# Optimization experiments

Measured on AMD Instinct MI355X. Metric: run time of the kernel, lower is better.

## Reference

```python
import jax, jax.numpy as jnp
import numpy as np

B, E, N = 8, 256, 32          # triples, padded edges per triple, neighbors per edge
D, RD = 512, 768              # graph_dim, relation-semantic dim
R = 2000                      # num relations
L = 2                         # relation-context layers
K = 8                         # top_k neighbor similarity
M, HEADS = 32, 8              # memory tokens, memory-attention heads
HLLM = 4096                   # llm hidden size
EPS = 1e-5


def _ln(x, g, b):
    mu = jnp.mean(x, -1, keepdims=True)
    var = jnp.mean(jnp.square(x - mu), -1, keepdims=True)
    return (x - mu) * jax.lax.rsqrt(var + EPS) * g + b


def setup_inputs() -> dict:
    key = jax.random.key(0)
    ks = iter(jax.random.split(key, 40))
    nrm = lambda shape, s=0.02: jax.random.normal(next(ks), shape, jnp.float32) * s
    return {
        'edge_rel_ids': jax.random.randint(next(ks), (B, E), 0, R, jnp.int32),
        'neighbor_rel_ids': jax.random.randint(next(ks), (B, E, N), 0, R, jnp.int32),
        'edge_mask': jnp.ones((B, E), jnp.float32),
        'rel_emb': nrm((R, RD), 1.0),
        'rp_w': nrm((D, RD)), 'rp_b': jnp.zeros((D,), jnp.float32),
        'ly_vw': nrm((L, D, D)), 'ly_vb': jnp.zeros((L, D), jnp.float32),
        'ly_ow': nrm((L, D, D)), 'ly_ob': jnp.zeros((L, D), jnp.float32),
        'ly_n1g': jnp.ones((L, D), jnp.float32), 'ly_n1b': jnp.zeros((L, D), jnp.float32),
        'ly_n2g': jnp.ones((L, D), jnp.float32), 'ly_n2b': jnp.zeros((L, D), jnp.float32),
        'ly_w1': nrm((L, 4 * D, D)), 'ly_b1': jnp.zeros((L, 4 * D), jnp.float32),
        'ly_w2': nrm((L, D, 4 * D)), 'ly_b2': jnp.zeros((L, D), jnp.float32),
        'mem_q': nrm((M, D)),
        't_qw': nrm((D, D)), 't_qb': jnp.zeros((D,), jnp.float32),
        't_kw': nrm((D, D)), 't_kb': jnp.zeros((D,), jnp.float32),
        't_vw': nrm((D, D)), 't_vb': jnp.zeros((D,), jnp.float32),
        't_ow': nrm((D, D)), 't_ob': jnp.zeros((D,), jnp.float32),
        'proj_w': nrm((HLLM, D)), 'proj_b': jnp.zeros((HLLM,), jnp.float32),
    }


def reference(edge_rel_ids, neighbor_rel_ids, edge_mask, rel_emb, rp_w, rp_b,
              ly_vw, ly_vb, ly_ow, ly_ob, ly_n1g, ly_n1b, ly_n2g, ly_n2b,
              ly_w1, ly_b1, ly_w2, ly_b2, mem_q,
              t_qw, t_qb, t_kw, t_kb, t_vw, t_vb, t_ow, t_ob, proj_w, proj_b):
    rel_vector = lambda ids: rel_emb[ids] @ rp_w.T + rp_b  # embedding gather + rel_proj
    rel_vec = rel_vector(edge_rel_ids)            # [B,E,D]
    neigh = rel_vector(neighbor_rel_ids)          # [B,E,N,D] dominant gather traffic
    # per-edge cosine similarity to neighbor relations, top-k mean aggregation
    rn = rel_vec / jnp.maximum(jnp.linalg.norm(rel_vec, axis=-1, keepdims=True), 1e-12)
    nn_ = neigh / jnp.maximum(jnp.linalg.norm(neigh, axis=-1, keepdims=True), 1e-12)
    sims = jnp.einsum('bend,bed->ben', nn_, rn)   # [B,E,N]
    _, top_idx = jax.lax.top_k(sims, K)           # [B,E,K]
    agg = jnp.take_along_axis(neigh, top_idx[..., None], axis=2).mean(axis=2)  # [B,E,D]
    # RelationContextLayer stack. Each layer attends from one edge-state token to a
    # single context token: softmax over one key is identically 1, so the MHA
    # reduces exactly to out_proj(v_proj(context)) -- same math as torch MHA here.
    states = rel_vec
    for l in range(L):
        attn = (agg @ ly_vw[l].T + ly_vb[l]) @ ly_ow[l].T + ly_ob[l]
        states = _ln(states + attn, ly_n1g[l], ly_n1b[l])
        ff = jax.nn.gelu(states @ ly_w1[l].T + ly_b1[l], approximate=False) @ ly_w2[l].T + ly_b2[l]
        states = _ln(states + ff, ly_n2g[l], ly_n2b[l])
        states = states * edge_mask[..., None]
    # GraphMemoryTokenizer: learned queries cross-attend over padded edge states
    dh = D // HEADS
    q = (mem_q @ t_qw.T + t_qb).reshape(M, HEADS, dh)
    k = (states @ t_kw.T + t_kb).reshape(B, E, HEADS, dh)
    v = (states @ t_vw.T + t_vb).reshape(B, E, HEADS, dh)
    scores = jnp.einsum('mhd,behd->bhme', q, k) / jnp.sqrt(jnp.asarray(dh, q.dtype))
    scores = jnp.where(edge_mask[:, None, None, :] == 0, jnp.finfo(scores.dtype).min, scores)
    attnw = jax.nn.softmax(scores, axis=-1)
    mem = jnp.einsum('bhme,behd->bmhd', attnw, v).reshape(B, M, D)
    mem = mem @ t_ow.T + t_ob
    no_edges = jnp.sum(edge_mask, axis=1) == 0    # rows with zero edges -> zero memory
    mem = jnp.where(no_edges[:, None, None], 0.0, mem)
    return mem @ proj_w.T + proj_b                # [B,M,HLLM]
```

## Files before the change

kernel.cpp:

```cpp
#include <hip/hip_runtime.h>
#include <hip/hip_bf16.h>
#include <math.h>

#define B_   8
#define E_   256
#define N_   32
#define D_   512
#define RD_  768
#define R_   2000
#define L_   2
#define K_   8
#define M_   32
#define H_   8
#define DH_  64
#define HL_  4096

typedef float f32x4 __attribute__((ext_vector_type(4)));
typedef __bf16 bf16x8 __attribute__((ext_vector_type(8)));
typedef const __attribute__((address_space(1))) void GVoid;
typedef __attribute__((address_space(3))) void LVoid;

__device__ __forceinline__ float gelu_exact(float x) {
    return 0.5f * x * (1.0f + erff(x * 0.70710678118654752f));
}
__device__ __forceinline__ unsigned short f2bf(float x) {
    return __hip_bfloat16_raw(__float2bfloat16(x)).x;
}

template <int TM, int TN, int ACT_GELU, int OUT_BF16, int HAS_BIAS, int FLAGS, int SPLITK = 1>
__global__ __launch_bounds__(256) void gemm_mfma(const unsigned short* __restrict__ A,
                                                 const unsigned short* __restrict__ W,
                                                 const float* __restrict__ bias,
                                                 void* __restrict__ Cv,
                                                 int M, int N, int K,
                                                 const float* __restrict__ rowflag) {
    constexpr int WTM = TM / 2, WTN = TN / 2;
    constexpr int RM = WTM / 16, RN = WTN / 16;
    constexpr int AI = TM / 32, BI = TN / 32;
    __shared__ __align__(16) unsigned short As[2 * TM * 64];
    __shared__ __align__(16) unsigned short Bs[2 * TN * 64];

    const int tid = threadIdx.x;
    const int wave = tid >> 6, lane = tid & 63;
    const int quad = lane >> 4, l16 = lane & 15;
    const int wm = wave >> 1, wn = wave & 1;
    const int bm = blockIdx.y * TM, bn = blockIdx.x * TN;
    const int bz = (SPLITK > 1) ? blockIdx.z : 0;
    const int sub = lane >> 3;
    const int cpr = (lane & 7) ^ sub;

    f32x4 acc[RM][RN];
#pragma unroll
    for (int i = 0; i < RM; i++)
#pragma unroll
        for (int j = 0; j < RN; j++) acc[i][j] = (f32x4){0.f, 0.f, 0.f, 0.f};

    const int kspan = K / SPLITK;
    const int kb = bz * kspan;
    const int nt = kspan / 64;

    auto stage = [&](int k0, int buf) {
#pragma unroll
        for (int i = 0; i < AI; i++) {
            int r0 = (wave * AI + i) * 8;
            const unsigned short* g = A + (size_t)(bm + r0 + sub) * K + k0 + cpr * 8;
            __builtin_amdgcn_global_load_lds((GVoid*)g, (LVoid*)&As[buf * TM * 64 + r0 * 64], 16, 0, 0);
        }
#pragma unroll
        for (int i = 0; i < BI; i++) {
            int r0 = (wave * BI + i) * 8;
            const unsigned short* g = W + (size_t)(bn + r0 + sub) * K + k0 + cpr * 8;
            __builtin_amdgcn_global_load_lds((GVoid*)g, (LVoid*)&Bs[buf * TN * 64 + r0 * 64], 16, 0, 0);
        }
    };

    stage(kb, 0);
    __syncthreads();

    for (int t = 0; t < nt; t++) {
        const int cur = t & 1;
        if (t + 1 < nt) stage(kb + (t + 1) * 64, cur ^ 1);
#pragma unroll
        for (int h = 0; h < 2; h++) {
            bf16x8 af[RM], bf[RN];
#pragma unroll
            for (int i = 0; i < RM; i++) {
                int r = wm * WTM + i * 16 + l16;
                int ch = (h * 4 + quad) ^ (r & 7);
                af[i] = *(const bf16x8*)&As[cur * TM * 64 + r * 64 + ch * 8];
            }
#pragma unroll
            for (int j = 0; j < RN; j++) {
                int r = wn * WTN + j * 16 + l16;
                int ch = (h * 4 + quad) ^ (r & 7);
                bf[j] = *(const bf16x8*)&Bs[cur * TN * 64 + r * 64 + ch * 8];
            }
#pragma unroll
            for (int i = 0; i < RM; i++)
#pragma unroll
                for (int j = 0; j < RN; j++)
                    acc[i][j] = __builtin_amdgcn_mfma_f32_16x16x32_bf16(af[i], bf[j], acc[i][j], 0, 0, 0);
        }
        __syncthreads();
    }

    float* Cf = (float*)Cv + (size_t)bz * M * N;
#pragma unroll
    for (int i = 0; i < RM; i++) {
#pragma unroll
        for (int j = 0; j < RN; j++) {
            int c = bn + wn * WTN + j * 16 + l16;
            float bv = (HAS_BIAS && bz == 0) ? bias[c] : 0.f;
#pragma unroll
            for (int reg = 0; reg < 4; reg++) {
                int r = bm + wm * WTM + i * 16 + quad * 4 + reg;
                if (r < M) {
                    float v = acc[i][j][reg] + bv;
                    if (ACT_GELU) v = gelu_exact(v);
                    if (FLAGS) v *= rowflag[r >> 5];
                    if (OUT_BF16)
                        ((unsigned short*)Cv)[(size_t)r * N + c] = f2bf(v);
                    else
                        Cf[(size_t)r * N + c] = v;
                }
            }
        }
    }
}

__global__ __launch_bounds__(256) void projwfuse_kernel(
        const unsigned short* __restrict__ rel_bf, const unsigned short* __restrict__ rpw_bf,
        const float* __restrict__ rp_b, float* __restrict__ proj,
        const unsigned short* __restrict__ ow_bf, const unsigned short* __restrict__ vwT_bf,
        unsigned short* __restrict__ wfuse) {
    __shared__ __align__(16) unsigned short As[2 * 32 * 64];
    __shared__ __align__(16) unsigned short Bs[2 * 64 * 64];

    const unsigned short *A, *W;
    const float* bias;
    int Mg, Kg, bm, bn, obf;
    void* C;
    int t = blockIdx.x;
    if (t < 504) {
        A = rel_bf; W = rpw_bf; bias = rp_b; Mg = R_; Kg = RD_;
        C = proj; obf = 0; bn = (t & 7) * 64; bm = (t >> 3) * 32;
    } else {
        int u = t - 504, z = u >> 7, uu = u & 127;
        A = ow_bf + (size_t)z * 262144; W = vwT_bf + (size_t)z * 262144;
        bias = nullptr; Mg = 512; Kg = 512;
        C = wfuse + (size_t)z * 262144; obf = 1; bn = (uu & 7) * 64; bm = (uu >> 3) * 32;
    }

    const int tid = threadIdx.x;
    const int wave = tid >> 6, lane = tid & 63;
    const int quad = lane >> 4, l16 = lane & 15;
    const int wm = wave >> 1, wn = wave & 1;
    const int sub = lane >> 3;
    const int cpr = (lane & 7) ^ sub;

    f32x4 acc[2];
    acc[0] = (f32x4){0.f, 0.f, 0.f, 0.f};
    acc[1] = (f32x4){0.f, 0.f, 0.f, 0.f};

    auto stage = [&](int k0, int buf) {
        {
            int r0 = wave * 8;
            const unsigned short* g = A + (size_t)(bm + r0 + sub) * Kg + k0 + cpr * 8;
            __builtin_amdgcn_global_load_lds((GVoid*)g, (LVoid*)&As[buf * 32 * 64 + r0 * 64], 16, 0, 0);
        }
#pragma unroll
        for (int i = 0; i < 2; i++) {
            int r0 = (wave * 2 + i) * 8;
            const unsigned short* g = W + (size_t)(bn + r0 + sub) * Kg + k0 + cpr * 8;
            __builtin_amdgcn_global_load_lds((GVoid*)g, (LVoid*)&Bs[buf * 64 * 64 + r0 * 64], 16, 0, 0);
        }
    };

    const int nt = Kg / 64;
    stage(0, 0);
    __syncthreads();

    for (int tt = 0; tt < nt; tt++) {
        const int cur = tt & 1;
        if (tt + 1 < nt) stage((tt + 1) * 64, cur ^ 1);
#pragma unroll
        for (int h = 0; h < 2; h++) {
            bf16x8 af, bf[2];
            {
                int r = wm * 16 + l16;
                int ch = (h * 4 + quad) ^ (r & 7);
                af = *(const bf16x8*)&As[cur * 32 * 64 + r * 64 + ch * 8];
            }
#pragma unroll
            for (int j = 0; j < 2; j++) {
                int r = wn * 32 + j * 16 + l16;
                int ch = (h * 4 + quad) ^ (r & 7);
                bf[j] = *(const bf16x8*)&Bs[cur * 64 * 64 + r * 64 + ch * 8];
            }
#pragma unroll
            for (int j = 0; j < 2; j++)
                acc[j] = __builtin_amdgcn_mfma_f32_16x16x32_bf16(af, bf[j], acc[j], 0, 0, 0);
        }
        __syncthreads();
    }

#pragma unroll
    for (int j = 0; j < 2; j++) {
        int c = bn + wn * 32 + j * 16 + l16;
        float bv = bias ? bias[c] : 0.f;
#pragma unroll
        for (int reg = 0; reg < 4; reg++) {
            int r = bm + wm * 16 + quad * 4 + reg;
            if (r < Mg) {
                float v = acc[j][reg] + bv;
                if (obf)
                    ((unsigned short*)C)[(size_t)r * 512 + c] = f2bf(v);
                else
                    ((float*)C)[(size_t)r * 512 + c] = v;
            }
        }
    }
}

struct PrepArgs {
    const float* src[9];
    unsigned short* dst[9];
    int cum4[10];
    int nb_cvt, total4;
    const float* ly_vw; unsigned short* vwT;
    const float* ly_ow; const float* ly_vb; const float* ly_ob; float* bfuse;
    const float* t_kb; const float* t_vb; float* kvb;
    const float* edge_mask; float* flags;
    const float* mem_q; const float* t_qw; const float* t_qb; float* qbuf;
};

__global__ __launch_bounds__(256) void prep_all(PrepArgs a) {
    int bx = blockIdx.x, tid = threadIdx.x;
    if (bx < a.nb_cvt) {
        int i = bx * 256 + tid;
        if (i < a.total4) {
            int k = 0;
#pragma unroll
            for (int j = 0; j < 8; j++) if (i >= a.cum4[j + 1]) k = j + 1;
            int o = i - a.cum4[k];
            float4 v = ((const float4*)a.src[k])[o];
            ushort4 u;
            u.x = f2bf(v.x); u.y = f2bf(v.y); u.z = f2bf(v.z); u.w = f2bf(v.w);
            ((ushort4*)a.dst[k])[o] = u;
        }
        return;
    }
    bx -= a.nb_cvt;
    if (bx < 512) {
        __shared__ float tile[32][33];
        int l = bx >> 8, t16 = bx & 255;
        int j0 = (t16 >> 4) * 32, k0 = (t16 & 15) * 32;
        int tx = tid & 31, ty = tid >> 5;
        const float* src = a.ly_vw + (size_t)l * 512 * 512;
        for (int r = ty; r < 32; r += 8)
            tile[r][tx] = src[(size_t)(j0 + r) * 512 + k0 + tx];
        __syncthreads();
        unsigned short* dst = a.vwT + (size_t)l * 512 * 512;
        for (int r = ty; r < 32; r += 8)
            dst[(size_t)(k0 + r) * 512 + j0 + tx] = f2bf(tile[tx][r]);
        return;
    }
    bx -= 512;
    if (bx < 256) {
        int wid = bx * 4 + (tid >> 6);
        int z = wid >> 9, n = wid & 511, lane = tid & 63;
        const float* owr = a.ly_ow + (size_t)z * 512 * 512 + (size_t)n * 512;
        const float* vbr = a.ly_vb + (size_t)z * 512;
        float s = 0.f;
#pragma unroll
        for (int j = 0; j < 8; j++) s += owr[lane + 64 * j] * vbr[lane + 64 * j];
#pragma unroll
        for (int off = 32; off; off >>= 1) s += __shfl_xor(s, off, 64);
        if (lane == 0) a.bfuse[z * 512 + n] = s + a.ly_ob[z * 512 + n];
        return;
    }
    bx -= 256;
    if (bx < 1) {
        __shared__ float red[4];
        for (int n = tid; n < 512; n += 256) {
            a.kvb[n] = a.t_kb[n];
            a.kvb[n + 512] = a.t_vb[n];
        }
        for (int b = 0; b < B_; b++) {
            float s = a.edge_mask[b * E_ + tid];
#pragma unroll
            for (int off = 32; off; off >>= 1) s += __shfl_xor(s, off, 64);
            if ((tid & 63) == 0) red[tid >> 6] = s;
            __syncthreads();
            if (tid == 0)
                a.flags[b] = (red[0] + red[1] + red[2] + red[3] == 0.f) ? 0.f : 1.f;
            __syncthreads();
        }
        return;
    }
    bx -= 1;
    {
        int wid = bx * 4 + (tid >> 6);
        int m = wid >> 9, n = wid & 511, lane = tid & 63;
        const float* ar = a.mem_q + (size_t)m * 512;
        const float* br = a.t_qw + (size_t)n * 512;
        float s = 0.f;
#pragma unroll
        for (int j = 0; j < 8; j++) s += ar[lane + 64 * j] * br[lane + 64 * j];
#pragma unroll
        for (int off = 32; off; off >>= 1) s += __shfl_xor(s, off, 64);
        if (lane == 0) a.qbuf[(size_t)m * 512 + n] = s + a.t_qb[n];
    }
}

__global__ void sim_topk_agg(const int* __restrict__ eids, const int* __restrict__ nids,
                             const float* __restrict__ proj,
                             unsigned short* __restrict__ agg_bf, float* __restrict__ states) {
    int be = blockIdx.x, tid = threadIdx.x;
    __shared__ float ev[512];
    __shared__ float sims[32];
    __shared__ int nid_s[32];
    __shared__ int sel[8];

    int eid = eids[be];
    const float* ep = proj + (size_t)eid * D_;
    float e0 = ep[tid], e1 = ep[tid + 256];
    ev[tid] = e0; ev[tid + 256] = e1;
    states[(size_t)be * D_ + tid] = e0;
    states[(size_t)be * D_ + tid + 256] = e1;
    if (tid < 32) nid_s[tid] = nids[be * N_ + tid];
    __syncthreads();

    int wid = tid >> 6, lane = tid & 63;
    float se = 0.f;
#pragma unroll
    for (int j = 0; j < 8; j++) { float v = ev[lane + 64 * j]; se += v * v; }
#pragma unroll
    for (int off = 32; off; off >>= 1) se += __shfl_xor(se, off, 64);
    float en = fmaxf(sqrtf(se), 1e-12f);

    for (int n = wid; n < N_; n += 4) {
        int nid = nid_s[n];
        const float* np = proj + (size_t)nid * D_;
        float s = 0.f, s2 = 0.f;
#pragma unroll
        for (int j = 0; j < 8; j++) {
            float v = np[lane + 64 * j];
            s += v * ev[lane + 64 * j];
            s2 += v * v;
        }
#pragma unroll
        for (int off = 32; off; off >>= 1) {
            s += __shfl_xor(s, off, 64);
            s2 += __shfl_xor(s2, off, 64);
        }
        if (lane == 0) sims[n] = s / (fmaxf(sqrtf(s2), 1e-12f) * en);
    }
    __syncthreads();

    if (tid < 64) {
        float v = (tid < 32) ? sims[tid] : -3.402823466e38f;
        int idx = tid;
        for (int k = 0; k < K_; k++) {
            float bv = v; int bi = idx;
#pragma unroll
            for (int off = 32; off; off >>= 1) {
                float ov = __shfl_xor(bv, off, 64);
                int oi = __shfl_xor(bi, off, 64);
                if (ov > bv || (ov == bv && oi < bi)) { bv = ov; bi = oi; }
            }
            if (tid == 0) sel[k] = nid_s[bi];
            if (idx == bi) v = -3.402823466e38f;
        }
    }
    __syncthreads();

    float a0 = 0.f, a1 = 0.f;
#pragma unroll
    for (int k = 0; k < K_; k++) {
        const float* sp = proj + (size_t)sel[k] * D_;
        a0 += sp[tid]; a1 += sp[tid + 256];
    }
    agg_bf[(size_t)be * D_ + tid] = f2bf(a0 * 0.125f);
    agg_bf[(size_t)be * D_ + tid + 256] = f2bf(a1 * 0.125f);
}

__global__ void add_ln_kernel(const float* __restrict__ x, const float* __restrict__ y,
                              int ystride, const float* __restrict__ y2,
                              const float* __restrict__ g,
                              const float* __restrict__ bb, const float* __restrict__ mask,
                              float* __restrict__ out, unsigned short* __restrict__ out_bf) {
    int t = blockIdx.x, tid = threadIdx.x;
    const float* xr = x + (size_t)t * D_;
    const float* yr = y + (size_t)t * ystride;
    float x0 = xr[tid] + yr[tid];
    float x1 = xr[tid + 256] + yr[tid + 256];
    if (y2) {
        const float* y2r = y2 + (size_t)t * D_;
        x0 += y2r[tid];
        x1 += y2r[tid + 256];
    }
    __shared__ float red[8];
    float s = x0 + x1;
#pragma unroll
    for (int off = 32; off; off >>= 1) s += __shfl_xor(s, off, 64);
    int wid = tid >> 6;
    if ((tid & 63) == 0) red[wid] = s;
    __syncthreads();
    float mean = (red[0] + red[1] + red[2] + red[3]) * (1.f / 512.f);
    float d0 = x0 - mean, d1 = x1 - mean;
    float v = d0 * d0 + d1 * d1;
#pragma unroll
    for (int off = 32; off; off >>= 1) v += __shfl_xor(v, off, 64);
    if ((tid & 63) == 0) red[4 + wid] = v;
    __syncthreads();
    float var = (red[4] + red[5] + red[6] + red[7]) * (1.f / 512.f);
    float rs = rsqrtf(var + 1e-5f);
    float mv = mask ? mask[t] : 1.f;
    float o0 = (d0 * rs * g[tid] + bb[tid]) * mv;
    float o1 = (d1 * rs * g[tid + 256] + bb[tid + 256]) * mv;
    out[(size_t)t * D_ + tid] = o0;
    out[(size_t)t * D_ + tid + 256] = o1;
    out_bf[(size_t)t * D_ + tid] = f2bf(o0);
    out_bf[(size_t)t * D_ + tid + 256] = f2bf(o1);
}

__global__ void dbl_ln_kernel(const float* __restrict__ x, const float* __restrict__ y,
                              const float* __restrict__ y2,
                              const float* __restrict__ g2, const float* __restrict__ b2,
                              const float* __restrict__ mask,
                              const float* __restrict__ att, int astride,
                              const float* __restrict__ g1, const float* __restrict__ b1,
                              float* __restrict__ out, unsigned short* __restrict__ out_bf) {
    int t = blockIdx.x, tid = threadIdx.x;
    const float* xr = x + (size_t)t * D_;
    const float* yr = y + (size_t)t * D_;
    float x0 = xr[tid] + yr[tid];
    float x1 = xr[tid + 256] + yr[tid + 256];
    if (y2) {
        const float* y2r = y2 + (size_t)t * D_;
        x0 += y2r[tid];
        x1 += y2r[tid + 256];
    }
    __shared__ float red[8];
    int wid = tid >> 6;
    float s = x0 + x1;
#pragma unroll
    for (int off = 32; off; off >>= 1) s += __shfl_xor(s, off, 64);
    if ((tid & 63) == 0) red[wid] = s;
    __syncthreads();
    float mean = (red[0] + red[1] + red[2] + red[3]) * (1.f / 512.f);
    float d0 = x0 - mean, d1 = x1 - mean;
    float v = d0 * d0 + d1 * d1;
#pragma unroll
    for (int off = 32; off; off >>= 1) v += __shfl_xor(v, off, 64);
    if ((tid & 63) == 0) red[4 + wid] = v;
    __syncthreads();
    float var = (red[4] + red[5] + red[6] + red[7]) * (1.f / 512.f);
    float rs = rsqrtf(var + 1e-5f);
    float mv = mask[t];
    float t0 = (d0 * rs * g2[tid] + b2[tid]) * mv;
    float t1 = (d1 * rs * g2[tid + 256] + b2[tid + 256]) * mv;
    const float* ar = att + (size_t)t * astride;
    float y0 = t0 + ar[tid];
    float y1 = t1 + ar[tid + 256];
    __syncthreads();
    float s2 = y0 + y1;
#pragma unroll
    for (int off = 32; off; off >>= 1) s2 += __shfl_xor(s2, off, 64);
    if ((tid & 63) == 0) red[wid] = s2;
    __syncthreads();
    float mean2 = (red[0] + red[1] + red[2] + red[3]) * (1.f / 512.f);
    float e0 = y0 - mean2, e1 = y1 - mean2;
    float v2 = e0 * e0 + e1 * e1;
#pragma unroll
    for (int off = 32; off; off >>= 1) v2 += __shfl_xor(v2, off, 64);
    if ((tid & 63) == 0) red[4 + wid] = v2;
    __syncthreads();
    float var2 = (red[4] + red[5] + red[6] + red[7]) * (1.f / 512.f);
    float rs2 = rsqrtf(var2 + 1e-5f);
    float o0 = e0 * rs2 * g1[tid] + b1[tid];
    float o1 = e1 * rs2 * g1[tid + 256] + b1[tid + 256];
    out[(size_t)t * D_ + tid] = o0;
    out[(size_t)t * D_ + tid + 256] = o1;
    out_bf[(size_t)t * D_ + tid] = f2bf(o0);
    out_bf[(size_t)t * D_ + tid + 256] = f2bf(o1);
}

__global__ void mem_attn(const float* __restrict__ qb, const float* __restrict__ kv,
                         const float* __restrict__ mask, unsigned short* __restrict__ memb) {
    int idx = blockIdx.x;
    int b = idx & 7;
    int h = (idx >> 3) & 7;
    int m = idx >> 6;
    int tid = threadIdx.x;
    __shared__ float qh[64];
    __shared__ float sc[256];
    __shared__ float red[8];
    __shared__ float oacc[4][64];

    float mk = mask[b * E_ + tid];
    if (tid < 64) qh[tid] = qb[m * D_ + h * DH_ + tid];
    __syncthreads();
    const float* kr = kv + ((size_t)(b * E_ + tid)) * 1024 + h * DH_;
    float s = 0.f;
#pragma unroll
    for (int d = 0; d < DH_; d += 4) {
        float4 k4 = *(const float4*)(kr + d);
        s += k4.x * qh[d] + k4.y * qh[d + 1] + k4.z * qh[d + 2] + k4.w * qh[d + 3];
    }
    s *= 0.125f;
    if (mk == 0.f) s = -3.402823466e38f;
    float mx = s;
#pragma unroll
    for (int off = 32; off; off >>= 1) mx = fmaxf(mx, __shfl_xor(mx, off, 64));
    if ((tid & 63) == 0) red[tid >> 6] = mx;
    __syncthreads();
    mx = fmaxf(fmaxf(red[0], red[1]), fmaxf(red[2], red[3]));
    float p = expf(s - mx);
    float sum = p;
#pragma unroll
    for (int off = 32; off; off >>= 1) sum += __shfl_xor(sum, off, 64);
    if ((tid & 63) == 0) red[4 + (tid >> 6)] = sum;
    __syncthreads();
    sum = red[4] + red[5] + red[6] + red[7];
    sc[tid] = p / sum;
    __syncthreads();
    int d = tid & 63, part = tid >> 6;
    const float* vcol = kv + ((size_t)(b * E_ + part * 64)) * 1024 + 512 + h * DH_ + d;
    float acc = 0.f;
#pragma unroll 8
    for (int e = 0; e < 64; e++) acc += sc[part * 64 + e] * vcol[(size_t)e * 1024];
    oacc[part][d] = acc;
    __syncthreads();
    if (part == 0)
        memb[((size_t)(b * M_ + m)) * D_ + h * DH_ + d] =
            f2bf(oacc[0][d] + oacc[1][d] + oacc[2][d] + oacc[3][d]);
}

extern "C" void kernel_launch(void* const* d_in, const int* in_sizes, int n_in,
                              void* d_out, int out_size, void* d_ws, size_t ws_size,
                              hipStream_t stream) {
    const int*   edge_rel_ids     = (const int*)d_in[0];
    const int*   neighbor_rel_ids = (const int*)d_in[1];
    const float* edge_mask        = (const float*)d_in[2];
    const float* rel_emb          = (const float*)d_in[3];
    const float* rp_w             = (const float*)d_in[4];
    const float* rp_b             = (const float*)d_in[5];
    const float* ly_vw            = (const float*)d_in[6];
    const float* ly_vb            = (const float*)d_in[7];
    const float* ly_ow            = (const float*)d_in[8];
    const float* ly_ob            = (const float*)d_in[9];
    const float* ly_n1g           = (const float*)d_in[10];
    const float* ly_n1b           = (const float*)d_in[11];
    const float* ly_n2g           = (const float*)d_in[12];
    const float* ly_n2b           = (const float*)d_in[13];
    const float* ly_w1            = (const float*)d_in[14];
    const float* ly_b1            = (const float*)d_in[15];
    const float* ly_w2            = (const float*)d_in[16];
    const float* ly_b2            = (const float*)d_in[17];
    const float* mem_q            = (const float*)d_in[18];
    const float* t_qw             = (const float*)d_in[19];
    const float* t_qb             = (const float*)d_in[20];
    const float* t_kw             = (const float*)d_in[21];
    const float* t_kb             = (const float*)d_in[22];
    const float* t_vw             = (const float*)d_in[23];
    const float* t_vb             = (const float*)d_in[24];
    const float* t_ow             = (const float*)d_in[25];
    const float* t_ob             = (const float*)d_in[26];
    const float* proj_w           = (const float*)d_in[27];
    const float* proj_b           = (const float*)d_in[28];
    float* out = (float*)d_out;
    (void)ws_size; (void)in_sizes; (void)n_in; (void)out_size;

    char* ws = (char*)d_ws;
    size_t off = 0;
    auto allocf = [&](size_t n) { float* p = (float*)(ws + off); off += ((n * 4 + 255) & ~(size_t)255); return p; };
    auto allocb = [&](size_t n) { unsigned short* p = (unsigned short*)(ws + off); off += ((n * 2 + 255) & ~(size_t)255); return p; };

    const int T = B_ * E_;

    float* states  = allocf((size_t)T * D_);
    float* statesX = allocf((size_t)T * D_);
    float* proj    = allocf((size_t)R_ * D_);
    float* tmpB    = allocf((size_t)T * D_ * 2);
    float* attnall = allocf((size_t)T * 2 * D_);
    float* qbuf    = allocf((size_t)M_ * D_);
    float* bfuse   = allocf(2 * D_);
    float* kvb     = allocf(2 * D_);
    float* flags   = allocf(B_);
    float* kvbuf   = attnall;

    unsigned short* rel_bf  = allocb((size_t)2048 * RD_);
    unsigned short* rpw_bf  = allocb((size_t)D_ * RD_);
    unsigned short* agg_bf  = allocb((size_t)T * D_);
    unsigned short* st_bf   = allocb((size_t)T * D_);
    unsigned short* ff1_bf  = allocb((size_t)T * 4 * D_);
    unsigned short* vwT_bf  = allocb((size_t)L_ * D_ * D_);
    unsigned short* ow_bf   = allocb((size_t)L_ * D_ * D_);
    unsigned short* wfuse   = allocb((size_t)L_ * D_ * D_);
    unsigned short* w1_bf   = allocb((size_t)L_ * 4 * D_ * D_);
    unsigned short* w2_bf   = allocb((size_t)L_ * 4 * D_ * D_);
    unsigned short* kvw_bf  = allocb((size_t)2 * D_ * D_);
    unsigned short* tow_bf  = allocb((size_t)D_ * D_);
    unsigned short* pw_bf   = allocb((size_t)HL_ * D_);
    unsigned short* memb_bf = allocb((size_t)B_ * M_ * D_);
    unsigned short* mem2_bf = allocb((size_t)B_ * M_ * D_);

    PrepArgs a;
    int sizes[9] = { R_ * RD_, D_ * RD_, L_ * D_ * D_, L_ * 4 * D_ * D_,
                     L_ * 4 * D_ * D_, D_ * D_, D_ * D_, D_ * D_, HL_ * D_ };
    const float* srcs[9] = { rel_emb, rp_w, ly_ow, ly_w1, ly_w2, t_kw, t_vw, t_ow, proj_w };
    unsigned short* dsts[9] = { rel_bf, rpw_bf, ow_bf, w1_bf, w2_bf,
                                kvw_bf, kvw_bf + (size_t)D_ * D_, tow_bf, pw_bf };
    int cum = 0;
    for (int i = 0; i < 9; i++) {
        a.src[i] = srcs[i]; a.dst[i] = dsts[i];
        a.cum4[i] = cum; cum += sizes[i] / 4;
    }
    a.cum4[9] = cum;
    a.total4 = cum;
    a.nb_cvt = (cum + 255) / 256;
    a.ly_vw = ly_vw; a.vwT = vwT_bf;
    a.ly_ow = ly_ow; a.ly_vb = ly_vb; a.ly_ob = ly_ob; a.bfuse = bfuse;
    a.t_kb = t_kb; a.t_vb = t_vb; a.kvb = kvb;
    a.edge_mask = edge_mask; a.flags = flags;
    a.mem_q = mem_q; a.t_qw = t_qw; a.t_qb = t_qb; a.qbuf = qbuf;
    int nblk = a.nb_cvt + 512 + 256 + 1 + 4096;
    prep_all<<<nblk, 256, 0, stream>>>(a);

    projwfuse_kernel<<<760, 256, 0, stream>>>(rel_bf, rpw_bf, rp_b, proj,
                                              ow_bf, vwT_bf, wfuse);

    sim_topk_agg<<<T, 256, 0, stream>>>(edge_rel_ids, neighbor_rel_ids, proj,
                                        agg_bf, states);

    gemm_mfma<64, 64, 0, 0, 1, 0><<<dim3(16, 32), 256, 0, stream>>>(
        agg_bf, wfuse, bfuse, attnall, T, 2 * D_, D_, nullptr);

    add_ln_kernel<<<T, 256, 0, stream>>>(states, attnall, 2 * D_, nullptr,
                                         ly_n1g, ly_n1b, nullptr, statesX, st_bf);
    gemm_mfma<64, 128, 1, 1, 1, 0><<<dim3(16, 32), 256, 0, stream>>>(
        st_bf, w1_bf, ly_b1, ff1_bf, T, 4 * D_, D_, nullptr);
    gemm_mfma<64, 64, 0, 0, 1, 0, 2><<<dim3(8, 32, 2), 256, 0, stream>>>(
        ff1_bf, w2_bf, ly_b2, tmpB, T, D_, 4 * D_, nullptr);
    dbl_ln_kernel<<<T, 256, 0, stream>>>(statesX, tmpB, tmpB + (size_t)T * D_,
                                         ly_n2g, ly_n2b, edge_mask,
                                         attnall + D_, 2 * D_, ly_n1g + D_, ly_n1b + D_,
                                         states, st_bf);
    gemm_mfma<64, 128, 1, 1, 1, 0><<<dim3(16, 32), 256, 0, stream>>>(
        st_bf, w1_bf + (size_t)4 * D_ * D_, ly_b1 + 4 * D_, ff1_bf, T, 4 * D_, D_, nullptr);
    gemm_mfma<64, 64, 0, 0, 1, 0, 2><<<dim3(8, 32, 2), 256, 0, stream>>>(
        ff1_bf, w2_bf + (size_t)4 * D_ * D_, ly_b2 + D_, tmpB, T, D_, 4 * D_, nullptr);
    add_ln_kernel<<<T, 256, 0, stream>>>(states, tmpB, D_, tmpB + (size_t)T * D_,
                                         ly_n2g + D_, ly_n2b + D_, edge_mask,
                                         statesX, st_bf);
    gemm_mfma<64, 64, 0, 0, 1, 0><<<dim3(16, 32), 256, 0, stream>>>(
        st_bf, kvw_bf, kvb, kvbuf, T, 2 * D_, D_, nullptr);
    mem_attn<<<B_ * M_ * H_, 256, 0, stream>>>(qbuf, kvbuf, edge_mask, memb_bf);
    gemm_mfma<32, 64, 0, 1, 1, 1><<<dim3(8, 8), 256, 0, stream>>>(
        memb_bf, tow_bf, t_ob, mem2_bf, B_ * M_, D_, D_, flags);
    gemm_mfma<32, 64, 0, 0, 1, 0><<<dim3(64, 8), 256, 0, stream>>>(
        mem2_bf, pw_bf, proj_b, out, B_ * M_, HL_, D_, nullptr);
}
```

Measured before the change: 307.2 us.

## Batch memory-attention queries per block and retune FFN GEMM tiling and split-K

The memory-attention kernel now handles 8 memory queries per block, so each K row and V column loaded serves 8 queries. This cuts redundant reads of the KV buffer and launches 8x fewer blocks. The FFN up-projection GEMMs switch to 64x64 tiles on a wider grid, and the down-projection moves from split-K 2 to 4, with the LayerNorm kernels summing a variable number of partial buffers. The last LayerNorm also skips its unused fp32 output store. The cost is more partial-sum traffic from split-K and higher register and shared-memory use in the attention kernel.

```diff
diff --git a/kernel.cpp b/kernel.cpp
--- a/kernel.cpp
+++ b/kernel.cpp
@@ -14,6 +14,7 @@
 #define H_   8
 #define DH_  64
 #define HL_  4096
+#define T_   2048
 
 typedef float f32x4 __attribute__((ext_vector_type(4)));
 typedef __bf16 bf16x8 __attribute__((ext_vector_type(8)));
@@ -386,7 +387,7 @@
 }
 
 __global__ void add_ln_kernel(const float* __restrict__ x, const float* __restrict__ y,
-                              int ystride, const float* __restrict__ y2,
+                              int ystride, const float* __restrict__ extra, int nextra,
                               const float* __restrict__ g,
                               const float* __restrict__ bb, const float* __restrict__ mask,
                               float* __restrict__ out, unsigned short* __restrict__ out_bf) {
@@ -395,10 +396,10 @@
     const float* yr = y + (size_t)t * ystride;
     float x0 = xr[tid] + yr[tid];
     float x1 = xr[tid + 256] + yr[tid + 256];
-    if (y2) {
-        const float* y2r = y2 + (size_t)t * D_;
-        x0 += y2r[tid];
-        x1 += y2r[tid + 256];
+    for (int j = 0; j < nextra; j++) {
+        const float* er = extra + (size_t)j * T_ * D_ + (size_t)t * D_;
+        x0 += er[tid];
+        x1 += er[tid + 256];
     }
     __shared__ float red[8];
     float s = x0 + x1;
@@ -419,14 +420,16 @@
     float mv = mask ? mask[t] : 1.f;
     float o0 = (d0 * rs * g[tid] + bb[tid]) * mv;
     float o1 = (d1 * rs * g[tid + 256] + bb[tid + 256]) * mv;
-    out[(size_t)t * D_ + tid] = o0;
-    out[(size_t)t * D_ + tid + 256] = o1;
+    if (out) {
+        out[(size_t)t * D_ + tid] = o0;
+        out[(size_t)t * D_ + tid + 256] = o1;
+    }
     out_bf[(size_t)t * D_ + tid] = f2bf(o0);
     out_bf[(size_t)t * D_ + tid + 256] = f2bf(o1);
 }
 
 __global__ void dbl_ln_kernel(const float* __restrict__ x, const float* __restrict__ y,
-                              const float* __restrict__ y2,
+                              const float* __restrict__ extra, int nextra,
                               const float* __restrict__ g2, const float* __restrict__ b2,
                               const float* __restrict__ mask,
                               const float* __restrict__ att, int astride,
@@ -437,10 +440,10 @@
     const float* yr = y + (size_t)t * D_;
     float x0 = xr[tid] + yr[tid];
     float x1 = xr[tid + 256] + yr[tid + 256];
-    if (y2) {
-        const float* y2r = y2 + (size_t)t * D_;
-        x0 += y2r[tid];
-        x1 += y2r[tid + 256];
+    for (int j = 0; j < nextra; j++) {
+        const float* er = extra + (size_t)j * T_ * D_ + (size_t)t * D_;
+        x0 += er[tid];
+        x1 += er[tid + 256];
     }
     __shared__ float red[8];
     int wid = tid >> 6;
@@ -492,50 +495,89 @@
     int idx = blockIdx.x;
     int b = idx & 7;
     int h = (idx >> 3) & 7;
-    int m = idx >> 6;
+    int mg = idx >> 6;
     int tid = threadIdx.x;
-    __shared__ float qh[64];
-    __shared__ float sc[256];
-    __shared__ float red[8];
-    __shared__ float oacc[4][64];
-
+    __shared__ float qh[8][64];
+    __shared__ float sc[8][256];
+    __shared__ float redm[4][8];
+    __shared__ float reds[4][8];
+    __shared__ float oacc[4][8][64];
+
+    for (int i = tid; i < 512; i += 256)
+        qh[i >> 6][i & 63] = qb[(size_t)(mg * 8 + (i >> 6)) * D_ + h * DH_ + (i & 63)];
     float mk = mask[b * E_ + tid];
-    if (tid < 64) qh[tid] = qb[m * D_ + h * DH_ + tid];
-    __syncthreads();
+    __syncthreads();
+
     const float* kr = kv + ((size_t)(b * E_ + tid)) * 1024 + h * DH_;
-    float s = 0.f;
+    float s[8];
+#pragma unroll
+    for (int i = 0; i < 8; i++) s[i] = 0.f;
 #pragma unroll
     for (int d = 0; d < DH_; d += 4) {
         float4 k4 = *(const float4*)(kr + d);
-        s += k4.x * qh[d] + k4.y * qh[d + 1] + k4.z * qh[d + 2] + k4.w * qh[d + 3];
-    }
-    s *= 0.125f;
-    if (mk == 0.f) s = -3.402823466e38f;
-    float mx = s;
-#pragma unroll
-    for (int off = 32; off; off >>= 1) mx = fmaxf(mx, __shfl_xor(mx, off, 64));
-    if ((tid & 63) == 0) red[tid >> 6] = mx;
-    __syncthreads();
-    mx = fmaxf(fmaxf(red[0], red[1]), fmaxf(red[2], red[3]));
-    float p = expf(s - mx);
-    float sum = p;
-#pragma unroll
-    for (int off = 32; off; off >>= 1) sum += __shfl_xor(sum, off, 64);
-    if ((tid & 63) == 0) red[4 + (tid >> 6)] = sum;
-    __syncthreads();
-    sum = red[4] + red[5] + red[6] + red[7];
-    sc[tid] = p / sum;
-    __syncthreads();
+#pragma unroll
+        for (int i = 0; i < 8; i++)
+            s[i] += k4.x * qh[i][d] + k4.y * qh[i][d + 1] + k4.z * qh[i][d + 2] + k4.w * qh[i][d + 3];
+    }
+#pragma unroll
+    for (int i = 0; i < 8; i++) {
+        s[i] *= 0.125f;
+        if (mk == 0.f) s[i] = -3.402823466e38f;
+    }
+
+    int wid = tid >> 6;
+    float m[8];
+#pragma unroll
+    for (int i = 0; i < 8; i++) m[i] = s[i];
+#pragma unroll
+    for (int off = 32; off; off >>= 1)
+#pragma unroll
+        for (int i = 0; i < 8; i++) m[i] = fmaxf(m[i], __shfl_xor(m[i], off, 64));
+    if ((tid & 63) == 0)
+#pragma unroll
+        for (int i = 0; i < 8; i++) redm[wid][i] = m[i];
+    __syncthreads();
+#pragma unroll
+    for (int i = 0; i < 8; i++)
+        m[i] = fmaxf(fmaxf(redm[0][i], redm[1][i]), fmaxf(redm[2][i], redm[3][i]));
+    float p[8], u[8];
+#pragma unroll
+    for (int i = 0; i < 8; i++) { p[i] = expf(s[i] - m[i]); u[i] = p[i]; }
+#pragma unroll
+    for (int off = 32; off; off >>= 1)
+#pragma unroll
+        for (int i = 0; i < 8; i++) u[i] += __shfl_xor(u[i], off, 64);
+    if ((tid & 63) == 0)
+#pragma unroll
+        for (int i = 0; i < 8; i++) reds[wid][i] = u[i];
+    __syncthreads();
+#pragma unroll
+    for (int i = 0; i < 8; i++) {
+        u[i] = reds[0][i] + reds[1][i] + reds[2][i] + reds[3][i];
+        sc[i][tid] = p[i] / u[i];
+    }
+    __syncthreads();
+
     int d = tid & 63, part = tid >> 6;
     const float* vcol = kv + ((size_t)(b * E_ + part * 64)) * 1024 + 512 + h * DH_ + d;
-    float acc = 0.f;
-#pragma unroll 8
-    for (int e = 0; e < 64; e++) acc += sc[part * 64 + e] * vcol[(size_t)e * 1024];
-    oacc[part][d] = acc;
-    __syncthreads();
-    if (part == 0)
-        memb[((size_t)(b * M_ + m)) * D_ + h * DH_ + d] =
-            f2bf(oacc[0][d] + oacc[1][d] + oacc[2][d] + oacc[3][d]);
+    float acc[8];
+#pragma unroll
+    for (int i = 0; i < 8; i++) acc[i] = 0.f;
+#pragma unroll 4
+    for (int e = 0; e < 64; e++) {
+        float vv = vcol[(size_t)e * 1024];
+#pragma unroll
+        for (int i = 0; i < 8; i++) acc[i] += sc[i][part * 64 + e] * vv;
+    }
+#pragma unroll
+    for (int i = 0; i < 8; i++) oacc[part][i][d] = acc[i];
+    __syncthreads();
+    if (part == 0) {
+#pragma unroll
+        for (int i = 0; i < 8; i++)
+            memb[((size_t)(b * M_ + mg * 8 + i)) * D_ + h * DH_ + d] =
+                f2bf(oacc[0][i][d] + oacc[1][i][d] + oacc[2][i][d] + oacc[3][i][d]);
+    }
 }
 
 extern "C" void kernel_launch(void* const* d_in, const int* in_sizes, int n_in,
@@ -583,7 +625,7 @@
     float* states  = allocf((size_t)T * D_);
     float* statesX = allocf((size_t)T * D_);
     float* proj    = allocf((size_t)R_ * D_);
-    float* tmpB    = allocf((size_t)T * D_ * 2);
+    float* tmpB    = allocf((size_t)T * D_ * 4);
     float* attnall = allocf((size_t)T * 2 * D_);
     float* qbuf    = allocf((size_t)M_ * D_);
     float* bfuse   = allocf(2 * D_);
@@ -638,26 +680,26 @@
     gemm_mfma<64, 64, 0, 0, 1, 0><<<dim3(16, 32), 256, 0, stream>>>(
         agg_bf, wfuse, bfuse, attnall, T, 2 * D_, D_, nullptr);
 
-    add_ln_kernel<<<T, 256, 0, stream>>>(states, attnall, 2 * D_, nullptr,
+    add_ln_kernel<<<T, 256, 0, stream>>>(states, attnall, 2 * D_, nullptr, 0,
                                          ly_n1g, ly_n1b, nullptr, statesX, st_bf);
-    gemm_mfma<64, 128, 1, 1, 1, 0><<<dim3(16, 32), 256, 0, stream>>>(
+    gemm_mfma<64, 64, 1, 1, 1, 0><<<dim3(32, 32), 256, 0, stream>>>(
         st_bf, w1_bf, ly_b1, ff1_bf, T, 4 * D_, D_, nullptr);
-    gemm_mfma<64, 64, 0, 0, 1, 0, 2><<<dim3(8, 32, 2), 256, 0, stream>>>(
+    gemm_mfma<64, 64, 0, 0, 1, 0, 4><<<dim3(8, 32, 4), 256, 0, stream>>>(
         ff1_bf, w2_bf, ly_b2, tmpB, T, D_, 4 * D_, nullptr);
-    dbl_ln_kernel<<<T, 256, 0, stream>>>(statesX, tmpB, tmpB + (size_t)T * D_,
+    dbl_ln_kernel<<<T, 256, 0, stream>>>(statesX, tmpB, tmpB + (size_t)T * D_, 3,
                                          ly_n2g, ly_n2b, edge_mask,
                                          attnall + D_, 2 * D_, ly_n1g + D_, ly_n1b + D_,
                                          states, st_bf);
-    gemm_mfma<64, 128, 1, 1, 1, 0><<<dim3(16, 32), 256, 0, stream>>>(
+    gemm_mfma<64, 64, 1, 1, 1, 0><<<dim3(32, 32), 256, 0, stream>>>(
         st_bf, w1_bf + (size_t)4 * D_ * D_, ly_b1 + 4 * D_, ff1_bf, T, 4 * D_, D_, nullptr);
-    gemm_mfma<64, 64, 0, 0, 1, 0, 2><<<dim3(8, 32, 2), 256, 0, stream>>>(
+    gemm_mfma<64, 64, 0, 0, 1, 0, 4><<<dim3(8, 32, 4), 256, 0, stream>>>(
         ff1_bf, w2_bf + (size_t)4 * D_ * D_, ly_b2 + D_, tmpB, T, D_, 4 * D_, nullptr);
-    add_ln_kernel<<<T, 256, 0, stream>>>(states, tmpB, D_, tmpB + (size_t)T * D_,
+    add_ln_kernel<<<T, 256, 0, stream>>>(states, tmpB, D_, tmpB + (size_t)T * D_, 3,
                                          ly_n2g + D_, ly_n2b + D_, edge_mask,
-                                         statesX, st_bf);
+                                         nullptr, st_bf);
     gemm_mfma<64, 64, 0, 0, 1, 0><<<dim3(16, 32), 256, 0, stream>>>(
         st_bf, kvw_bf, kvb, kvbuf, T, 2 * D_, D_, nullptr);
-    mem_attn<<<B_ * M_ * H_, 256, 0, stream>>>(qbuf, kvbuf, edge_mask, memb_bf);
+    mem_attn<<<B_ * H_ * (M_ / 8), 256, 0, stream>>>(qbuf, kvbuf, edge_mask, memb_bf);
     gemm_mfma<32, 64, 0, 1, 1, 1><<<dim3(8, 8), 256, 0, stream>>>(
         memb_bf, tow_bf, t_ob, mem2_bf, B_ * M_, D_, D_, flags);
     gemm_mfma<32, 64, 0, 0, 1, 0><<<dim3(64, 8), 256, 0, stream>>>(
```

New measurement: 296.6 us. -3.4%, faster.
